# Optimization experiments

Measured on AMD Instinct MI355X. Metric: run time of the kernel, lower is better.

## Reference

```python
import jax, jax.numpy as jnp
import numpy as np

N_NODES = 100000
N_EDGES = 1250000
HID = 64
IN_CH = 64
OUT_CH = 16
N_GRAPHS = 512


def setup_inputs() -> dict:
    key = jax.random.key(0)
    ks = jax.random.split(key, 20)
    x = jax.random.normal(ks[0], (N_NODES, IN_CH), dtype=jnp.float32)
    edge_index = jax.random.randint(ks[1], (2, N_EDGES), 0, N_NODES, dtype=jnp.int64)
    batch = jnp.sort(jax.random.randint(ks[2], (N_NODES,), 0, N_GRAPHS, dtype=jnp.int64))
    s_in = 1.0 / np.sqrt(IN_CH)
    s_h = 1.0 / np.sqrt(HID)
    u = lambda k, shp, s: jax.random.uniform(k, shp, jnp.float32, -s, s)
    return {
        "x": x, "edge_index": edge_index, "batch": batch,
        "W0": u(ks[3], (IN_CH, HID), s_in), "b0": u(ks[4], (HID,), s_in),
        "W1a": u(ks[5], (HID, HID), s_h), "b1a": u(ks[6], (HID,), s_h),
        "W1b": u(ks[7], (HID, HID), s_h), "b1b": u(ks[8], (HID,), s_h),
        "W2a": u(ks[9], (HID, HID), s_h), "b2a": u(ks[10], (HID,), s_h),
        "W2b": u(ks[11], (HID, HID), s_h), "b2b": u(ks[12], (HID,), s_h),
        "W3a": u(ks[13], (HID, HID), s_h), "b3a": u(ks[14], (HID,), s_h),
        "W3b": u(ks[15], (HID, HID), s_h), "b3b": u(ks[16], (HID,), s_h),
        "Wl": u(ks[17], (HID, OUT_CH), s_h), "bl": u(ks[18], (OUT_CH,), s_h),
    }


def _gin_conv(h, src, dst, Wa, ba, Wb, bb):
    # GINConv, eps=0: mlp(x_i + sum_{j->i} x_j); mlp = Linear,ReLU,Linear
    agg = jax.ops.segment_sum(h[src], dst, num_segments=N_NODES)  # [N, HID]
    z = h + agg
    return jax.nn.relu(z @ Wa + ba) @ Wb + bb


def reference(x, edge_index, batch, W0, b0, W1a, b1a, W1b, b1b,
              W2a, b2a, W2b, b2b, W3a, b3a, W3b, b3b, Wl, bl):
    src, dst = edge_index[0], edge_index[1]
    h = jax.nn.relu(x @ W0 + b0)
    h = jax.nn.relu(_gin_conv(h, src, dst, W1a, b1a, W1b, b1b))
    h = jax.nn.relu(_gin_conv(h, src, dst, W2a, b2a, W2b, b2b))
    h = jax.nn.relu(_gin_conv(h, src, dst, W3a, b3a, W3b, b3b))
    # global mean pool over graphs
    sums = jax.ops.segment_sum(h, batch, num_segments=N_GRAPHS)  # [G, HID]
    cnts = jax.ops.segment_sum(jnp.ones((N_NODES,), h.dtype), batch, num_segments=N_GRAPHS)
    pooled = sums / jnp.maximum(cnts, 1.0)[:, None]
    # dropout p=0.5 is identity in eval mode
    return pooled @ Wl + bl  # [G, OUT_CH]
```

## Files before the change

### kernel.cpp

```cpp
#include <hip/hip_runtime.h>
#include <hip/hip_fp16.h>

#define N_NODES 100000
#define N_EDGES 1250000
#define HID 64
#define N_GRAPHS 512
#define OUT_CH 16

#define BK_NODES 64
#define NBUCKET ((N_NODES + BK_NODES - 1) / BK_NODES)
#define NREP 8
#define SEG_CAP 192
#define BK_STRIDE (NREP * SEG_CAP)
#define TILE1 ((N_NODES + 63) / 64)
#define TSTRIDE 68

typedef _Float16 h16;
typedef _Float16 half2_t __attribute__((ext_vector_type(2)));
typedef _Float16 f16x8 __attribute__((ext_vector_type(8)));
typedef float f32x4 __attribute__((ext_vector_type(4)));

__device__ __forceinline__ void acc4(uint2 u, float& a0, float& a1, float& a2, float& a3) {
    half2_t h0 = __builtin_bit_cast(half2_t, u.x);
    half2_t h1 = __builtin_bit_cast(half2_t, u.y);
    a0 += (float)h0[0];
    a1 += (float)h0[1];
    a2 += (float)h1[0];
    a3 += (float)h1[1];
}

__device__ __forceinline__ unsigned pack2(float x, float y) {
    half2_t o;
    o[0] = (h16)x;
    o[1] = (h16)y;
    return __builtin_bit_cast(unsigned, o);
}

__global__ __launch_bounds__(256) void k_partition(const int* __restrict__ src,
                                                   const int* __restrict__ dst,
                                                   int* __restrict__ cnt,
                                                   int* __restrict__ buckets) {
    int i = blockIdx.x * 256 + threadIdx.x;
    if (i >= N_EDGES) return;
    int rep = blockIdx.x & (NREP - 1);
    int s = src[i];
    int d = dst[i];
    int b = d >> 6;
    int pos = atomicAdd(&cnt[b * NREP + rep], 1);
    if (pos < SEG_CAP)
        buckets[(size_t)b * BK_STRIDE + rep * SEG_CAP + pos] = ((d & 63) << 17) | s;
}

__global__ __launch_bounds__(256) void k_bucket_sort(const int* __restrict__ cnt,
                                                     int* __restrict__ buckets,
                                                     int* __restrict__ rowptrL) {
    __shared__ int srt[BK_STRIDE];
    __shared__ int hist[BK_NODES];
    __shared__ int curs[BK_NODES];
    int b = blockIdx.x, t = threadIdx.x;
    int* gb = buckets + (size_t)b * BK_STRIDE;
    int c[NREP];
#pragma unroll
    for (int r = 0; r < NREP; ++r) {
        int x = cnt[b * NREP + r];
        c[r] = x < SEG_CAP ? x : SEG_CAP;
    }
    if (t < BK_NODES) hist[t] = 0;
    __syncthreads();
#pragma unroll
    for (int r = 0; r < NREP; ++r)
        for (int i = t; i < c[r]; i += 256)
            atomicAdd(&hist[gb[r * SEG_CAP + i] >> 17], 1);
    __syncthreads();
    if (t < 64) {
        int h = hist[t];
        int x = h;
        for (int off = 1; off < 64; off <<= 1) {
            int u = __shfl_up(x, off, 64);
            if (t >= off) x += u;
        }
        curs[t] = x - h;
        rowptrL[b * 65 + t] = x - h;
        if (t == 63) rowptrL[b * 65 + 64] = x;
    }
    __syncthreads();
#pragma unroll
    for (int r = 0; r < NREP; ++r)
        for (int i = t; i < c[r]; i += 256) {
            int rec = gb[r * SEG_CAP + i];
            int pos = atomicAdd(&curs[rec >> 17], 1);
            srt[pos] = rec;
        }
    __syncthreads();
    int n = 0;
#pragma unroll
    for (int r = 0; r < NREP; ++r) n += c[r];
    for (int i = t; i < n; i += 256) gb[i] = srt[i];
}

__global__ __launch_bounds__(256) void k_aggregate(const int* __restrict__ rowptrL,
                                                   const int* __restrict__ buckets,
                                                   const h16* __restrict__ H,
                                                   h16* __restrict__ Z) {
    const uint2* H4 = (const uint2*)H;
    uint2* Z4 = (uint2*)Z;
    int lane = threadIdx.x & 63;
    int part = lane >> 4, sub = lane & 15;
    int gwave = (blockIdx.x * 256 + threadIdx.x) >> 6;
    int nw = (gridDim.x * 256) >> 6;
    for (int i0 = gwave * 4; i0 < N_NODES; i0 += nw * 4) {
        int i = i0 + part;
        bool valid = i < N_NODES;
        int iv = valid ? i : N_NODES - 1;
        int b = iv >> 6, local = iv & 63;
        int start = rowptrL[b * 65 + local];
        int end = valid ? rowptrL[b * 65 + local + 1] : start;
        const int* bk = buckets + (size_t)b * BK_STRIDE;
        float a0 = 0.f, a1 = 0.f, a2 = 0.f, a3 = 0.f;
        acc4(H4[(size_t)iv * 16 + sub], a0, a1, a2, a3);
        int j = start;
        for (; j + 8 <= end; j += 8) {
            int s0 = bk[j] & 0x1FFFF;
            int s1 = bk[j + 1] & 0x1FFFF;
            int s2 = bk[j + 2] & 0x1FFFF;
            int s3 = bk[j + 3] & 0x1FFFF;
            int s4 = bk[j + 4] & 0x1FFFF;
            int s5 = bk[j + 5] & 0x1FFFF;
            int s6 = bk[j + 6] & 0x1FFFF;
            int s7 = bk[j + 7] & 0x1FFFF;
            uint2 u0 = H4[(size_t)s0 * 16 + sub];
            uint2 u1 = H4[(size_t)s1 * 16 + sub];
            uint2 u2 = H4[(size_t)s2 * 16 + sub];
            uint2 u3 = H4[(size_t)s3 * 16 + sub];
            uint2 u4 = H4[(size_t)s4 * 16 + sub];
            uint2 u5 = H4[(size_t)s5 * 16 + sub];
            uint2 u6 = H4[(size_t)s6 * 16 + sub];
            uint2 u7 = H4[(size_t)s7 * 16 + sub];
            acc4(u0, a0, a1, a2, a3);
            acc4(u1, a0, a1, a2, a3);
            acc4(u2, a0, a1, a2, a3);
            acc4(u3, a0, a1, a2, a3);
            acc4(u4, a0, a1, a2, a3);
            acc4(u5, a0, a1, a2, a3);
            acc4(u6, a0, a1, a2, a3);
            acc4(u7, a0, a1, a2, a3);
        }
        if (j + 4 <= end) {
            int s0 = bk[j] & 0x1FFFF;
            int s1 = bk[j + 1] & 0x1FFFF;
            int s2 = bk[j + 2] & 0x1FFFF;
            int s3 = bk[j + 3] & 0x1FFFF;
            uint2 u0 = H4[(size_t)s0 * 16 + sub];
            uint2 u1 = H4[(size_t)s1 * 16 + sub];
            uint2 u2 = H4[(size_t)s2 * 16 + sub];
            uint2 u3 = H4[(size_t)s3 * 16 + sub];
            acc4(u0, a0, a1, a2, a3);
            acc4(u1, a0, a1, a2, a3);
            acc4(u2, a0, a1, a2, a3);
            acc4(u3, a0, a1, a2, a3);
            j += 4;
        }
        if (j + 2 <= end) {
            int s0 = bk[j] & 0x1FFFF;
            int s1 = bk[j + 1] & 0x1FFFF;
            uint2 u0 = H4[(size_t)s0 * 16 + sub];
            uint2 u1 = H4[(size_t)s1 * 16 + sub];
            acc4(u0, a0, a1, a2, a3);
            acc4(u1, a0, a1, a2, a3);
            j += 2;
        }
        if (j < end) {
            int s = bk[j] & 0x1FFFF;
            acc4(H4[(size_t)s * 16 + sub], a0, a1, a2, a3);
        }
        if (valid) {
            uint2 o;
            o.x = pack2(a0, a1);
            o.y = pack2(a2, a3);
            Z4[(size_t)i * 16 + sub] = o;
        }
    }
}

__global__ __launch_bounds__(256) void k_wprep(const float* __restrict__ Wq0,
                                               const float* __restrict__ Wq1,
                                               const float* __restrict__ Wq2,
                                               const float* __restrict__ Wq3,
                                               const float* __restrict__ Wq4,
                                               const float* __restrict__ Wq5,
                                               const float* __restrict__ Wq6,
                                               h16* __restrict__ WF) {
    const float* Ws[7] = {Wq0, Wq1, Wq2, Wq3, Wq4, Wq5, Wq6};
    const float* W = Ws[blockIdx.x];
    h16* dstW = WF + (size_t)blockIdx.x * 4096;
    int t = threadIdx.x;
#pragma unroll
    for (int i = 0; i < 16; ++i) {
        int s = t + 256 * i;
        int k = s >> 6, col = s & 63;
        int kc = k >> 5, quad = (k >> 3) & 3, j = k & 7;
        int c = col >> 4, n = col & 15;
        dstW[((c * 2 + kc) * 4 + quad) * 128 + n * 8 + j] = (h16)W[s];
    }
}

__global__ __launch_bounds__(256) void k_mlp(const h16* __restrict__ WaF,
                                             const float* __restrict__ Ba,
                                             const h16* __restrict__ WbF,
                                             const float* __restrict__ Bb,
                                             const h16* __restrict__ Zin,
                                             h16* __restrict__ Hout) {
    __shared__ float sT[4 * 16 * TSTRIDE];
    int t = threadIdx.x;
    int w = t >> 6, lane = t & 63;
    int n16 = lane & 15, quad = lane >> 4;
    float* T = sT + w * 16 * TSTRIDE;
    int rbase = blockIdx.x * 64 + w * 16;

    int arow = rbase + n16;
    int crow = arow < N_NODES ? arow : N_NODES - 1;
    const f16x8* zp = (const f16x8*)(Zin + (size_t)crow * HID + quad * 8);
    f16x8 a0 = zp[0];
    f16x8 a1 = zp[4];

    f16x8 bwa[4][2], bwb[4][2];
#pragma unroll
    for (int c = 0; c < 4; ++c)
#pragma unroll
        for (int kc = 0; kc < 2; ++kc) {
            int f = ((c * 2 + kc) * 4 + quad) * 128 + n16 * 8;
            bwa[c][kc] = *(const f16x8*)(WaF + f);
            bwb[c][kc] = *(const f16x8*)(WbF + f);
        }

    f32x4 acc[4];
#pragma unroll
    for (int c = 0; c < 4; ++c) {
        float bv = Ba[c * 16 + n16];
        acc[c] = (f32x4){bv, bv, bv, bv};
        acc[c] = __builtin_amdgcn_mfma_f32_16x16x32_f16(a0, bwa[c][0], acc[c], 0, 0, 0);
        acc[c] = __builtin_amdgcn_mfma_f32_16x16x32_f16(a1, bwa[c][1], acc[c], 0, 0, 0);
    }

#pragma unroll
    for (int c = 0; c < 4; ++c)
#pragma unroll
        for (int r = 0; r < 4; ++r)
            T[(quad * 4 + r) * TSTRIDE + c * 16 + n16] = fmaxf(acc[c][r], 0.f);

    f16x8 ta[2];
#pragma unroll
    for (int kc = 0; kc < 2; ++kc) {
        float4 p = *(const float4*)&T[n16 * TSTRIDE + kc * 32 + quad * 8];
        float4 q = *(const float4*)&T[n16 * TSTRIDE + kc * 32 + quad * 8 + 4];
        f16x8 v;
        v[0] = (h16)p.x; v[1] = (h16)p.y; v[2] = (h16)p.z; v[3] = (h16)p.w;
        v[4] = (h16)q.x; v[5] = (h16)q.y; v[6] = (h16)q.z; v[7] = (h16)q.w;
        ta[kc] = v;
    }

#pragma unroll
    for (int c = 0; c < 4; ++c) {
        float bv = Bb[c * 16 + n16];
        acc[c] = (f32x4){bv, bv, bv, bv};
        acc[c] = __builtin_amdgcn_mfma_f32_16x16x32_f16(ta[0], bwb[c][0], acc[c], 0, 0, 0);
        acc[c] = __builtin_amdgcn_mfma_f32_16x16x32_f16(ta[1], bwb[c][1], acc[c], 0, 0, 0);
    }

#pragma unroll
    for (int c = 0; c < 4; ++c)
#pragma unroll
        for (int r = 0; r < 4; ++r)
            T[(quad * 4 + r) * TSTRIDE + c * 16 + n16] = fmaxf(acc[c][r], 0.f);
    {
        int rl = lane >> 2, seg = lane & 3;
        int row = rbase + rl;
        if (row < N_NODES) {
            const float* tr = &T[rl * TSTRIDE + seg * 16];
            f16x8 o0, o1;
#pragma unroll
            for (int i = 0; i < 8; ++i) {
                o0[i] = (h16)tr[i];
                o1[i] = (h16)tr[8 + i];
            }
            f16x8* dp = (f16x8*)(Hout + (size_t)row * HID + seg * 16);
            dp[0] = o0;
            dp[1] = o1;
        }
    }
}

__global__ __launch_bounds__(256) void k_lin(const h16* __restrict__ W0F,
                                             const float* __restrict__ B,
                                             const float* __restrict__ Xin,
                                             h16* __restrict__ Hout) {
    __shared__ float sT[4 * 16 * TSTRIDE];
    int t = threadIdx.x;
    int w = t >> 6, lane = t & 63;
    int n16 = lane & 15, quad = lane >> 4;
    float* T = sT + w * 16 * TSTRIDE;
    int rbase = blockIdx.x * 64 + w * 16;

    int arow = rbase + n16;
    int crow = arow < N_NODES ? arow : N_NODES - 1;
    f16x8 a[2];
#pragma unroll
    for (int kc = 0; kc < 2; ++kc) {
        const float4* xp = (const float4*)(Xin + (size_t)crow * HID + kc * 32 + quad * 8);
        float4 p = xp[0], q = xp[1];
        f16x8 v;
        v[0] = (h16)p.x; v[1] = (h16)p.y; v[2] = (h16)p.z; v[3] = (h16)p.w;
        v[4] = (h16)q.x; v[5] = (h16)q.y; v[6] = (h16)q.z; v[7] = (h16)q.w;
        a[kc] = v;
    }

    f32x4 acc[4];
#pragma unroll
    for (int c = 0; c < 4; ++c) {
        float bv = B[c * 16 + n16];
        acc[c] = (f32x4){bv, bv, bv, bv};
#pragma unroll
        for (int kc = 0; kc < 2; ++kc) {
            f16x8 bw = *(const f16x8*)(W0F + ((c * 2 + kc) * 4 + quad) * 128 + n16 * 8);
            acc[c] = __builtin_amdgcn_mfma_f32_16x16x32_f16(a[kc], bw, acc[c], 0, 0, 0);
        }
    }

#pragma unroll
    for (int c = 0; c < 4; ++c)
#pragma unroll
        for (int r = 0; r < 4; ++r)
            T[(quad * 4 + r) * TSTRIDE + c * 16 + n16] = fmaxf(acc[c][r], 0.f);
    {
        int rl = lane >> 2, seg = lane & 3;
        int row = rbase + rl;
        if (row < N_NODES) {
            const float* tr = &T[rl * TSTRIDE + seg * 16];
            f16x8 o0, o1;
#pragma unroll
            for (int i = 0; i < 8; ++i) {
                o0[i] = (h16)tr[i];
                o1[i] = (h16)tr[8 + i];
            }
            f16x8* dp = (f16x8*)(Hout + (size_t)row * HID + seg * 16);
            dp[0] = o0;
            dp[1] = o1;
        }
    }
}

__global__ __launch_bounds__(256) void k_poolfinal(const h16* __restrict__ H,
                                                   const int* __restrict__ batch,
                                                   const float* __restrict__ Wl,
                                                   const float* __restrict__ bl,
                                                   float* __restrict__ out) {
    __shared__ float sp[4 * HID];
    int g = blockIdx.x;
    int t = threadIdx.x;
    int lane = t & 63, w = t >> 6;
    int lo = 0, hi = N_NODES;
    while (lo < hi) { int m = (lo + hi) >> 1; if (batch[m] < g) lo = m + 1; else hi = m; }
    int start = lo;
    hi = N_NODES;
    while (lo < hi) { int m = (lo + hi) >> 1; if (batch[m] < g + 1) lo = m + 1; else hi = m; }
    int end = lo;
    float s = 0.f;
    for (int r = start + w; r < end; r += 4) s += (float)H[(size_t)r * HID + lane];
    sp[w * HID + lane] = s;
    __syncthreads();
    if (t < HID) {
        float tot = sp[t] + sp[HID + t] + sp[2 * HID + t] + sp[3 * HID + t];
        float c = (end > start) ? (float)(end - start) : 1.0f;
        sp[t] = tot / c;
    }
    __syncthreads();
    if (t < OUT_CH) {
        float acc = bl[t];
#pragma unroll
        for (int k = 0; k < HID; ++k) acc += sp[k] * Wl[k * OUT_CH + t];
        out[g * OUT_CH + t] = acc;
    }
}

extern "C" void kernel_launch(void* const* d_in, const int* in_sizes, int n_in,
                              void* d_out, int out_size, void* d_ws, size_t ws_size,
                              hipStream_t stream) {
    const float* x     = (const float*)d_in[0];
    const int*   edge  = (const int*)d_in[1];
    const int*   batch = (const int*)d_in[2];
    const float* W0  = (const float*)d_in[3];
    const float* b0  = (const float*)d_in[4];
    const float* W1a = (const float*)d_in[5];
    const float* b1a = (const float*)d_in[6];
    const float* W1b = (const float*)d_in[7];
    const float* b1b = (const float*)d_in[8];
    const float* W2a = (const float*)d_in[9];
    const float* b2a = (const float*)d_in[10];
    const float* W2b = (const float*)d_in[11];
    const float* b2b = (const float*)d_in[12];
    const float* W3a = (const float*)d_in[13];
    const float* b3a = (const float*)d_in[14];
    const float* W3b = (const float*)d_in[15];
    const float* b3b = (const float*)d_in[16];
    const float* Wl  = (const float*)d_in[17];
    const float* bl  = (const float*)d_in[18];
    float* out = (float*)d_out;

    const int* src = edge;
    const int* dst = edge + N_EDGES;

    h16* HA = (h16*)d_ws;
    h16* Z  = HA + (size_t)N_NODES * HID;
    int* cnt     = (int*)(Z + (size_t)N_NODES * HID);
    int* rowptrL = cnt + NBUCKET * NREP;
    int* buckets = rowptrL + NBUCKET * 65;
    h16* WF      = (h16*)(buckets + (size_t)NBUCKET * BK_STRIDE);
    h16* W0F = WF;
    h16* W1aF = WF + 4096 * 1;
    h16* W1bF = WF + 4096 * 2;
    h16* W2aF = WF + 4096 * 3;
    h16* W2bF = WF + 4096 * 4;
    h16* W3aF = WF + 4096 * 5;
    h16* W3bF = WF + 4096 * 6;

    hipMemsetAsync(cnt, 0, NBUCKET * NREP * sizeof(int), stream);
    k_partition<<<(N_EDGES + 255) / 256, 256, 0, stream>>>(src, dst, cnt, buckets);
    k_bucket_sort<<<NBUCKET, 256, 0, stream>>>(cnt, buckets, rowptrL);
    k_wprep<<<7, 256, 0, stream>>>(W0, W1a, W1b, W2a, W2b, W3a, W3b, WF);

    k_lin<<<TILE1, 256, 0, stream>>>(W0F, b0, x, HA);

    k_aggregate<<<6250, 256, 0, stream>>>(rowptrL, buckets, HA, Z);
    k_mlp<<<TILE1, 256, 0, stream>>>(W1aF, b1a, W1bF, b1b, Z, HA);

    k_aggregate<<<6250, 256, 0, stream>>>(rowptrL, buckets, HA, Z);
    k_mlp<<<TILE1, 256, 0, stream>>>(W2aF, b2a, W2bF, b2b, Z, HA);

    k_aggregate<<<6250, 256, 0, stream>>>(rowptrL, buckets, HA, Z);
    k_mlp<<<TILE1, 256, 0, stream>>>(W3aF, b3a, W3bF, b3b, Z, HA);

    k_poolfinal<<<N_GRAPHS, 256, 0, stream>>>(HA, batch, Wl, bl, out);
}
```

Baseline: 330.7 us.

## Replace per-edge global atomic bucketing with block-local counting-sort into 512-node superbuckets

Edge partitioning now builds a shared-memory histogram per 2048-edge block, reserves one contiguous range per superbucket with a single global atomic, and writes the staged records with vectorized stores. Superbuckets cover 512 destination nodes and hold up to 8192 edges. The sort kernel then orders each superbucket by local node and emits global row pointers. The goal is to cut global atomic contention and scattered writes in CSR construction. In exchange, each superbucket has a fixed capacity, so a very skewed destination distribution would silently drop edges.

```diff
diff --git a/kernel.cpp b/kernel.cpp
--- a/kernel.cpp
+++ b/kernel.cpp
@@ -7,11 +7,10 @@
 #define N_GRAPHS 512
 #define OUT_CH 16
 
-#define BK_NODES 64
-#define NBUCKET ((N_NODES + BK_NODES - 1) / BK_NODES)
-#define NREP 8
-#define SEG_CAP 192
-#define BK_STRIDE (NREP * SEG_CAP)
+#define NSUP 196
+#define SB_CAP 8192
+#define E_BLK 2048
+#define NPB ((N_EDGES + E_BLK - 1) / E_BLK)
 #define TILE1 ((N_NODES + 63) / 64)
 #define TSTRIDE 68
 
@@ -40,65 +39,109 @@
                                                    const int* __restrict__ dst,
                                                    int* __restrict__ cnt,
                                                    int* __restrict__ buckets) {
-    int i = blockIdx.x * 256 + threadIdx.x;
-    if (i >= N_EDGES) return;
-    int rep = blockIdx.x & (NREP - 1);
-    int s = src[i];
-    int d = dst[i];
-    int b = d >> 6;
-    int pos = atomicAdd(&cnt[b * NREP + rep], 1);
-    if (pos < SEG_CAP)
-        buckets[(size_t)b * BK_STRIDE + rep * SEG_CAP + pos] = ((d & 63) << 17) | s;
-}
-
-__global__ __launch_bounds__(256) void k_bucket_sort(const int* __restrict__ cnt,
-                                                     int* __restrict__ buckets,
-                                                     int* __restrict__ rowptrL) {
-    __shared__ int srt[BK_STRIDE];
-    __shared__ int hist[BK_NODES];
-    __shared__ int curs[BK_NODES];
-    int b = blockIdx.x, t = threadIdx.x;
-    int* gb = buckets + (size_t)b * BK_STRIDE;
-    int c[NREP];
-#pragma unroll
-    for (int r = 0; r < NREP; ++r) {
-        int x = cnt[b * NREP + r];
-        c[r] = x < SEG_CAP ? x : SEG_CAP;
-    }
-    if (t < BK_NODES) hist[t] = 0;
-    __syncthreads();
-#pragma unroll
-    for (int r = 0; r < NREP; ++r)
-        for (int i = t; i < c[r]; i += 256)
-            atomicAdd(&hist[gb[r * SEG_CAP + i] >> 17], 1);
-    __syncthreads();
-    if (t < 64) {
-        int h = hist[t];
-        int x = h;
-        for (int off = 1; off < 64; off <<= 1) {
-            int u = __shfl_up(x, off, 64);
-            if (t >= off) x += u;
-        }
-        curs[t] = x - h;
-        rowptrL[b * 65 + t] = x - h;
-        if (t == 63) rowptrL[b * 65 + 64] = x;
-    }
-    __syncthreads();
-#pragma unroll
-    for (int r = 0; r < NREP; ++r)
-        for (int i = t; i < c[r]; i += 256) {
-            int rec = gb[r * SEG_CAP + i];
-            int pos = atomicAdd(&curs[rec >> 17], 1);
-            srt[pos] = rec;
-        }
-    __syncthreads();
-    int n = 0;
-#pragma unroll
-    for (int r = 0; r < NREP; ++r) n += c[r];
+    __shared__ int hist[256];
+    __shared__ int gbase[256];
+    __shared__ int tsum[256];
+    __shared__ int stage[E_BLK];
+    int t = threadIdx.x;
+    int e0 = blockIdx.x * E_BLK;
+    int eN = N_EDGES - e0;
+    if (eN > E_BLK) eN = E_BLK;
+
+    hist[t] = 0;
+    __syncthreads();
+    for (int i = t; i < eN; i += 256) atomicAdd(&hist[dst[e0 + i] >> 9], 1);
+    __syncthreads();
+
+    int c = hist[t];
+    tsum[t] = c;
+    __syncthreads();
+    for (int off = 1; off < 256; off <<= 1) {
+        int u = (t >= off) ? tsum[t - off] : 0;
+        __syncthreads();
+        tsum[t] += u;
+        __syncthreads();
+    }
+    int pref = tsum[t] - c;
+    if (t < NSUP && c > 0) gbase[t] = atomicAdd(&cnt[t], c);
+    hist[t] = pref;
+    __syncthreads();
+
+    for (int i = t; i < eN; i += 256) {
+        int s = src[e0 + i];
+        int d = dst[e0 + i];
+        int p = atomicAdd(&hist[d >> 9], 1);
+        stage[p] = ((d & 511) << 17) | s;
+    }
+    __syncthreads();
+
+    if (t < NSUP && c > 0) {
+        int lstart = hist[t] - c;
+        int gb = gbase[t];
+        int cap = SB_CAP - gb;
+        int n = c < cap ? c : (cap > 0 ? cap : 0);
+        int* dp = buckets + (size_t)t * SB_CAP + gb;
+        int r = 0;
+        while (r < n && (((size_t)(dp + r)) & 15)) { dp[r] = stage[lstart + r]; ++r; }
+        for (; r + 4 <= n; r += 4) {
+            int4 v;
+            v.x = stage[lstart + r];
+            v.y = stage[lstart + r + 1];
+            v.z = stage[lstart + r + 2];
+            v.w = stage[lstart + r + 3];
+            *(int4*)(dp + r) = v;
+        }
+        for (; r < n; ++r) dp[r] = stage[lstart + r];
+    }
+}
+
+__global__ __launch_bounds__(256) void k_sort(const int* __restrict__ cnt,
+                                              int* __restrict__ buckets,
+                                              int* __restrict__ rowptrS) {
+    __shared__ int srt[SB_CAP];
+    __shared__ int hist[512];
+    __shared__ int curs[512];
+    __shared__ int tsum[256];
+    int s = blockIdx.x, t = threadIdx.x;
+    int n = cnt[s];
+    n = n < SB_CAP ? n : SB_CAP;
+    int* gb = buckets + (size_t)s * SB_CAP;
+    int sBase = s * SB_CAP;
+
+    hist[t] = 0;
+    hist[t + 256] = 0;
+    __syncthreads();
+    for (int i = t; i < n; i += 256) atomicAdd(&hist[gb[i] >> 17], 1);
+    __syncthreads();
+
+    int c0 = hist[2 * t], c1 = hist[2 * t + 1];
+    int tot = c0 + c1;
+    tsum[t] = tot;
+    __syncthreads();
+    for (int off = 1; off < 256; off <<= 1) {
+        int u = (t >= off) ? tsum[t - off] : 0;
+        __syncthreads();
+        tsum[t] += u;
+        __syncthreads();
+    }
+    int pref = tsum[t] - tot;
+    curs[2 * t] = pref;
+    curs[2 * t + 1] = pref + c0;
+    rowptrS[s * 513 + 2 * t] = sBase + pref;
+    rowptrS[s * 513 + 2 * t + 1] = sBase + pref + c0;
+    if (t == 255) rowptrS[s * 513 + 512] = sBase + n;
+    __syncthreads();
+
+    for (int i = t; i < n; i += 256) {
+        int rec = gb[i];
+        int pos = atomicAdd(&curs[rec >> 17], 1);
+        srt[pos] = rec;
+    }
+    __syncthreads();
     for (int i = t; i < n; i += 256) gb[i] = srt[i];
 }
 
-__global__ __launch_bounds__(256) void k_aggregate(const int* __restrict__ rowptrL,
+__global__ __launch_bounds__(256) void k_aggregate(const int* __restrict__ rowptrS,
                                                    const int* __restrict__ buckets,
                                                    const h16* __restrict__ H,
                                                    h16* __restrict__ Z) {
@@ -112,22 +155,21 @@
         int i = i0 + part;
         bool valid = i < N_NODES;
         int iv = valid ? i : N_NODES - 1;
-        int b = iv >> 6, local = iv & 63;
-        int start = rowptrL[b * 65 + local];
-        int end = valid ? rowptrL[b * 65 + local + 1] : start;
-        const int* bk = buckets + (size_t)b * BK_STRIDE;
+        int s = iv >> 9, l = iv & 511;
+        int start = rowptrS[s * 513 + l];
+        int end = valid ? rowptrS[s * 513 + l + 1] : start;
         float a0 = 0.f, a1 = 0.f, a2 = 0.f, a3 = 0.f;
         acc4(H4[(size_t)iv * 16 + sub], a0, a1, a2, a3);
         int j = start;
         for (; j + 8 <= end; j += 8) {
-            int s0 = bk[j] & 0x1FFFF;
-            int s1 = bk[j + 1] & 0x1FFFF;
-            int s2 = bk[j + 2] & 0x1FFFF;
-            int s3 = bk[j + 3] & 0x1FFFF;
-            int s4 = bk[j + 4] & 0x1FFFF;
-            int s5 = bk[j + 5] & 0x1FFFF;
-            int s6 = bk[j + 6] & 0x1FFFF;
-            int s7 = bk[j + 7] & 0x1FFFF;
+            int s0 = buckets[j] & 0x1FFFF;
+            int s1 = buckets[j + 1] & 0x1FFFF;
+            int s2 = buckets[j + 2] & 0x1FFFF;
+            int s3 = buckets[j + 3] & 0x1FFFF;
+            int s4 = buckets[j + 4] & 0x1FFFF;
+            int s5 = buckets[j + 5] & 0x1FFFF;
+            int s6 = buckets[j + 6] & 0x1FFFF;
+            int s7 = buckets[j + 7] & 0x1FFFF;
             uint2 u0 = H4[(size_t)s0 * 16 + sub];
             uint2 u1 = H4[(size_t)s1 * 16 + sub];
             uint2 u2 = H4[(size_t)s2 * 16 + sub];
@@ -146,10 +188,10 @@
             acc4(u7, a0, a1, a2, a3);
         }
         if (j + 4 <= end) {
-            int s0 = bk[j] & 0x1FFFF;
-            int s1 = bk[j + 1] & 0x1FFFF;
-            int s2 = bk[j + 2] & 0x1FFFF;
-            int s3 = bk[j + 3] & 0x1FFFF;
+            int s0 = buckets[j] & 0x1FFFF;
+            int s1 = buckets[j + 1] & 0x1FFFF;
+            int s2 = buckets[j + 2] & 0x1FFFF;
+            int s3 = buckets[j + 3] & 0x1FFFF;
             uint2 u0 = H4[(size_t)s0 * 16 + sub];
             uint2 u1 = H4[(size_t)s1 * 16 + sub];
             uint2 u2 = H4[(size_t)s2 * 16 + sub];
@@ -161,8 +203,8 @@
             j += 4;
         }
         if (j + 2 <= end) {
-            int s0 = bk[j] & 0x1FFFF;
-            int s1 = bk[j + 1] & 0x1FFFF;
+            int s0 = buckets[j] & 0x1FFFF;
+            int s1 = buckets[j + 1] & 0x1FFFF;
             uint2 u0 = H4[(size_t)s0 * 16 + sub];
             uint2 u1 = H4[(size_t)s1 * 16 + sub];
             acc4(u0, a0, a1, a2, a3);
@@ -170,8 +212,8 @@
             j += 2;
         }
         if (j < end) {
-            int s = bk[j] & 0x1FFFF;
-            acc4(H4[(size_t)s * 16 + sub], a0, a1, a2, a3);
+            int s0 = buckets[j] & 0x1FFFF;
+            acc4(H4[(size_t)s0 * 16 + sub], a0, a1, a2, a3);
         }
         if (valid) {
             uint2 o;
@@ -412,9 +454,9 @@
     h16* HA = (h16*)d_ws;
     h16* Z  = HA + (size_t)N_NODES * HID;
     int* cnt     = (int*)(Z + (size_t)N_NODES * HID);
-    int* rowptrL = cnt + NBUCKET * NREP;
-    int* buckets = rowptrL + NBUCKET * 65;
-    h16* WF      = (h16*)(buckets + (size_t)NBUCKET * BK_STRIDE);
+    int* rowptrS = cnt + NSUP;
+    int* buckets = rowptrS + NSUP * 513;
+    h16* WF      = (h16*)(buckets + (size_t)NSUP * SB_CAP);
     h16* W0F = WF;
     h16* W1aF = WF + 4096 * 1;
     h16* W1bF = WF + 4096 * 2;
@@ -423,20 +465,20 @@
     h16* W3aF = WF + 4096 * 5;
     h16* W3bF = WF + 4096 * 6;
 
-    hipMemsetAsync(cnt, 0, NBUCKET * NREP * sizeof(int), stream);
-    k_partition<<<(N_EDGES + 255) / 256, 256, 0, stream>>>(src, dst, cnt, buckets);
-    k_bucket_sort<<<NBUCKET, 256, 0, stream>>>(cnt, buckets, rowptrL);
+    hipMemsetAsync(cnt, 0, NSUP * sizeof(int), stream);
+    k_partition<<<NPB, 256, 0, stream>>>(src, dst, cnt, buckets);
+    k_sort<<<NSUP, 256, 0, stream>>>(cnt, buckets, rowptrS);
     k_wprep<<<7, 256, 0, stream>>>(W0, W1a, W1b, W2a, W2b, W3a, W3b, WF);
 
     k_lin<<<TILE1, 256, 0, stream>>>(W0F, b0, x, HA);
 
-    k_aggregate<<<6250, 256, 0, stream>>>(rowptrL, buckets, HA, Z);
+    k_aggregate<<<6250, 256, 0, stream>>>(rowptrS, buckets, HA, Z);
     k_mlp<<<TILE1, 256, 0, stream>>>(W1aF, b1a, W1bF, b1b, Z, HA);
 
-    k_aggregate<<<6250, 256, 0, stream>>>(rowptrL, buckets, HA, Z);
+    k_aggregate<<<6250, 256, 0, stream>>>(rowptrS, buckets, HA, Z);
     k_mlp<<<TILE1, 256, 0, stream>>>(W2aF, b2a, W2bF, b2b, Z, HA);
 
-    k_aggregate<<<6250, 256, 0, stream>>>(rowptrL, buckets, HA, Z);
+    k_aggregate<<<6250, 256, 0, stream>>>(rowptrS, buckets, HA, Z);
     k_mlp<<<TILE1, 256, 0, stream>>>(W3aF, b3a, W3bF, b3b, Z, HA);
 
     k_poolfinal<<<N_GRAPHS, 256, 0, stream>>>(HA, batch, Wl, bl, out);
```

Result: faster. 295.5 us (-10.6%).
